# Kernel optimization log

Measured on AMD Instinct MI355X. Metric: run time of the kernel, lower is better.

Reference implementation:

```python
import jax, jax.numpy as jnp
import numpy as np

EPS_BN = 1e-5
NEG_SLOPE = 0.2
N_GRAPHS = 64


def _gat_layer(x, src, dst, W, att_s, att_d, b, concat):
    # x: [N, Fin]; W: [Fin, H*C]; att_s/att_d: [H, C]; PyG GATConv semantics
    N = x.shape[0]
    H, C = att_s.shape
    h = (x @ W).reshape(N, H, C)                      # [N,H,C]
    a_s = jnp.einsum('nhc,hc->nh', h, att_s)          # per-node src score
    a_d = jnp.einsum('nhc,hc->nh', h, att_d)          # per-node dst score
    e = jax.nn.leaky_relu(a_s[src] + a_d[dst], NEG_SLOPE)  # [E,H]
    m = jax.ops.segment_max(e, dst, num_segments=N)   # segment softmax over incoming edges
    ex = jnp.exp(e - m[dst])
    den = jax.ops.segment_sum(ex, dst, num_segments=N)
    alpha = ex / (den[dst] + 1e-16)                   # [E,H]
    msg = h[src] * alpha[:, :, None]                  # [E,H,C]
    out = jax.ops.segment_sum(msg, dst, num_segments=N)
    out = out.reshape(N, H * C) if concat else out.mean(axis=1)
    return out + b


def _bn(x, g, bt):
    mu = x.mean(axis=0)
    var = x.var(axis=0)
    return (x - mu) * jax.lax.rsqrt(var + EPS_BN) * g + bt


def setup_inputs() -> dict:
    key = jax.random.key(0)
    ks = jax.random.split(key, 32)
    N, E, F = 50000, 800000, 128
    d = {}
    d['x'] = jax.random.normal(ks[0], (N, F), dtype=jnp.float32)
    d['edge_index'] = jax.random.randint(ks[1], (2, E), 0, N, dtype=jnp.int32)
    d['batch'] = jnp.sort(jax.random.randint(ks[2], (N,), 0, N_GRAPHS, dtype=jnp.int32))
    def p(k, shape, fan):
        return jax.random.normal(k, shape, dtype=jnp.float32) * (1.0 / np.sqrt(fan))
    d['W1'] = p(ks[3], (128, 256), 128); d['as1'] = p(ks[4], (4, 64), 64)
    d['ad1'] = p(ks[5], (4, 64), 64); d['b1'] = jnp.zeros((256,), jnp.float32)
    d['W2'] = p(ks[6], (256, 128), 256); d['as2'] = p(ks[7], (4, 32), 32)
    d['ad2'] = p(ks[8], (4, 32), 32); d['b2'] = jnp.zeros((128,), jnp.float32)
    # gat3: 128 -> 64, 1 head, mean
    d['W3'] = p(ks[9], (128, 64), 128); d['as3'] = p(ks[10], (1, 64), 64)
    d['ad3'] = p(ks[11], (1, 64), 64); d['b3'] = jnp.zeros((64,), jnp.float32)
    # batch norms
    d['g1'] = jnp.ones((256,), jnp.float32); d['bt1'] = jnp.zeros((256,), jnp.float32)
    d['g2'] = jnp.ones((128,), jnp.float32); d['bt2'] = jnp.zeros((128,), jnp.float32)
    d['g3'] = jnp.ones((64,), jnp.float32); d['bt3'] = jnp.zeros((64,), jnp.float32)
    # fcn: 64 -> 128 -> 32 -> 2
    d['fw1'] = p(ks[12], (64, 128), 64); d['fb1'] = jnp.zeros((128,), jnp.float32)
    d['fw2'] = p(ks[13], (128, 32), 128); d['fb2'] = jnp.zeros((32,), jnp.float32)
    d['fw3'] = p(ks[14], (32, 2), 32); d['fb3'] = jnp.zeros((2,), jnp.float32)
    return d


def reference(x, edge_index, batch, W1, as1, ad1, b1, W2, as2, ad2, b2,
              W3, as3, ad3, b3, g1, bt1, g2, bt2, g3, bt3,
              fw1, fb1, fw2, fb2, fw3, fb3):
    N = x.shape[0]
    # add self loops (PyG GATConv default)
    loops = jnp.arange(N, dtype=edge_index.dtype)
    src = jnp.concatenate([edge_index[0], loops])
    dst = jnp.concatenate([edge_index[1], loops])
    h = _gat_layer(x, src, dst, W1, as1, ad1, b1, concat=True)
    h = jax.nn.elu(_bn(h, g1, bt1))
    h = _gat_layer(h, src, dst, W2, as2, ad2, b2, concat=True)
    h = jax.nn.elu(_bn(h, g2, bt2))
    h = _gat_layer(h, src, dst, W3, as3, ad3, b3, concat=False)
    h = jax.nn.elu(_bn(h, g3, bt3))
    # global mean pool per graph
    s = jax.ops.segment_sum(h, batch, num_segments=N_GRAPHS)
    cnt = jax.ops.segment_sum(jnp.ones((N,), h.dtype), batch, num_segments=N_GRAPHS)
    pooled = s / jnp.maximum(cnt, 1.0)[:, None]       # [64, 64]
    z = jax.nn.leaky_relu(pooled @ fw1 + fb1, NEG_SLOPE)
    z = jax.nn.leaky_relu(z @ fw2 + fb2, NEG_SLOPE)
    return z @ fw3 + fb3                              # [64, 2]
```

## Files before the change

### kernel.cpp

```cpp
#include <hip/hip_runtime.h>
#include <hip/hip_fp16.h>
#include <math.h>

#define NEG_SLOPE 0.2f
#define BN_NB 128
#define BK_SHIFT 6
#define BK_CAP 2048
#define SC_CHUNK 4096

typedef _Float16 f16x8 __attribute__((ext_vector_type(8)));
typedef float    f32x4 __attribute__((ext_vector_type(4)));


__device__ inline void scan1024_incl(int* tmp) {
    int t = threadIdx.x;
    for (int off = 1; off < 1024; off <<= 1) {
        int vals[4];
#pragma unroll
        for (int k = 0; k < 4; k++) {
            int idx = t + k * 256;
            vals[k] = (idx >= off) ? tmp[idx - off] : 0;
        }
        __syncthreads();
#pragma unroll
        for (int k = 0; k < 4; k++) tmp[t + k * 256] += vals[k];
        __syncthreads();
    }
}

__global__ __launch_bounds__(256) void histA_kernel(const int* __restrict__ dst,
                                                    int* __restrict__ bcnt, int E, int nb) {
    __shared__ int h[1024];
    int t = threadIdx.x;
    for (int i = t; i < 1024; i += 256) h[i] = 0;
    __syncthreads();
    int base = blockIdx.x * SC_CHUNK;
#pragma unroll 4
    for (int k = 0; k < SC_CHUNK / 256; k++) {
        int i = base + t + k * 256;
        if (i < E) atomicAdd(&h[dst[i] >> BK_SHIFT], 1);
    }
    __syncthreads();
    for (int i = t; i < nb; i += 256) if (h[i]) atomicAdd(&bcnt[i], h[i]);
}

__global__ __launch_bounds__(256) void scanAB_kernel(const int* __restrict__ bcnt,
                                                     int* __restrict__ boffs,
                                                     int* __restrict__ gcurs, int nb) {
    __shared__ int tmp[1024];
    int t = threadIdx.x;
    for (int i = t; i < 1024; i += 256) tmp[i] = (i < nb) ? bcnt[i] : 0;
    __syncthreads();
    scan1024_incl(tmp);
    for (int i = t; i < nb; i += 256) {
        int excl = (i == 0) ? 0 : tmp[i - 1];
        boffs[i] = excl;
        gcurs[i] = excl;
    }
    if (t == 0) boffs[nb] = tmp[nb - 1];
}

__global__ __launch_bounds__(256) void scatterB_kernel(const int* __restrict__ src,
                                                       const int* __restrict__ dst,
                                                       int* __restrict__ gcurs,
                                                       unsigned* __restrict__ ebuf,
                                                       int E, int nb) {
    __shared__ int hcnt[1024];
    __shared__ int hcur[1024];
    __shared__ int gbase[1024];
    __shared__ unsigned stage[SC_CHUNK];
    __shared__ unsigned short sbk[SC_CHUNK];
    int t = threadIdx.x;
    int base = blockIdx.x * SC_CHUNK;
    for (int i = t; i < 1024; i += 256) hcnt[i] = 0;
    __syncthreads();
    unsigned pk[SC_CHUNK / 256];
    int bk[SC_CHUNK / 256];
#pragma unroll
    for (int k = 0; k < SC_CHUNK / 256; k++) {
        int i = base + t + k * 256;
        if (i < E) {
            int d = dst[i];
            int s = src[i];
            bk[k] = d >> BK_SHIFT;
            pk[k] = (unsigned)s | ((unsigned)(d & 63) << 16);
            atomicAdd(&hcnt[bk[k]], 1);
        } else bk[k] = -1;
    }
    __syncthreads();
    for (int i = t; i < 1024; i += 256) hcur[i] = hcnt[i];
    __syncthreads();
    scan1024_incl(hcur);
    for (int i = t; i < 1024; i += 256) hcur[i] -= hcnt[i];
    __syncthreads();
#pragma unroll
    for (int k = 0; k < SC_CHUNK / 256; k++) {
        if (bk[k] >= 0) {
            int p = atomicAdd(&hcur[bk[k]], 1);
            stage[p] = pk[k];
            sbk[p] = (unsigned short)bk[k];
        }
    }
    __syncthreads();
    for (int i = t; i < nb; i += 256) {
        int c = hcnt[i];
        gbase[i] = c ? atomicAdd(&gcurs[i], c) : 0;
    }
    __syncthreads();
    int total = E - base; if (total > SC_CHUNK) total = SC_CHUNK;
    for (int i = t; i < total; i += 256) {
        int b = sbk[i];
        int local = i - (hcur[b] - hcnt[b]);
        ebuf[gbase[b] + local] = stage[i];
    }
}

__global__ __launch_bounds__(256) void buildC_kernel(const unsigned* __restrict__ ebuf,
                                                     const int* __restrict__ boffs,
                                                     int* __restrict__ offs,
                                                     int* __restrict__ csrc, int N) {
    __shared__ int ncnt[64], ncur[64];
    __shared__ int npre[65];
    __shared__ unsigned lv[BK_CAP];
    __shared__ int lout[BK_CAP];
    int b = blockIdx.x, t = threadIdx.x;
    int e0 = boffs[b], e1 = boffs[b + 1];
    int cnt = e1 - e0; if (cnt > BK_CAP) cnt = BK_CAP;
    int n0 = b << BK_SHIFT;
    if (t < 64) ncnt[t] = 0;
    __syncthreads();
    for (int i = t; i < cnt; i += 256) {
        unsigned v = ebuf[e0 + i];
        lv[i] = v;
        atomicAdd(&ncnt[v >> 16], 1);
    }
    __syncthreads();
    if (t == 0) {
        int run = 0;
#pragma unroll
        for (int i = 0; i < 64; i++) { npre[i] = run; run += ncnt[i]; }
        npre[64] = run;
    }
    __syncthreads();
    int nEnd = N - n0; if (nEnd > 64) nEnd = 64;
    if (t < nEnd) offs[n0 + t + 1] = e0 + npre[t + 1];
    if (b == 0 && t == 0) offs[0] = 0;
    if (t < 64) ncur[t] = npre[t];
    __syncthreads();
    for (int i = t; i < cnt; i += 256) {
        unsigned v = lv[i];
        int p = atomicAdd(&ncur[v >> 16], 1);
        lout[p] = (int)(v & 0xFFFFu);
    }
    __syncthreads();
    for (int i = t; i < cnt; i += 256) csrc[e0 + i] = lout[i];
}


__device__ inline void swz1(const float* __restrict__ W, __half* __restrict__ Wsw,
                            int Nout, int i) {
    int k = i / Nout, n = i % Nout;
    Wsw[((size_t)(k >> 3) * Nout + n) * 8 + (k & 7)] = __float2half(W[i]);
}

__global__ void prep_kernel(const float* __restrict__ W1, const float* __restrict__ W2,
                            const float* __restrict__ W3,
                            const float* __restrict__ as1, const float* __restrict__ ad1,
                            __half* __restrict__ W1sw, __half* __restrict__ W2sw,
                            __half* __restrict__ W3sw, float* __restrict__ wsd,
                            const float* __restrict__ x, __half* __restrict__ Xh,
                            int castN4) {
    int i = blockIdx.x * 256 + threadIdx.x;
    const int R0 = 128 * 256, R1 = R0 + 256 * 128, R2 = R1 + 128 * 64, R3 = R2 + 1024;
    if (i < R0) { swz1(W1, W1sw, 256, i); }
    else if (i < R1) { swz1(W2, W2sw, 128, i - R0); }
    else if (i < R2) { swz1(W3, W3sw, 64, i - R1); }
    else if (i < R3) {
        int j = (i - R2) >> 7, k = (i - R2) & 127;
        int hh = j & 3;
        const float* att = (j < 4) ? as1 : ad1;
        float s = 0.f;
        for (int c = 0; c < 64; c++) s += W1[k * 256 + hh * 64 + c] * att[hh * 64 + c];
        wsd[i - R2] = s;
    } else {
        int j = i - R3;
        if (j < castN4) {
            float4 v = *(const float4*)(x + (size_t)j * 4);
            __half2 pk[2];
            pk[0] = __floats2half2_rn(v.x, v.y);
            pk[1] = __floats2half2_rn(v.z, v.w);
            *(uint2*)(Xh + (size_t)j * 4) = *(uint2*)pk;
        }
    }
}


__global__ __launch_bounds__(256) void scores1_kernel(const __half* __restrict__ Xh,
                                                      const float* __restrict__ wsd,
                                                      float* __restrict__ a_s,
                                                      float* __restrict__ a_d, int N) {
    int gid = blockIdx.x * 256 + threadIdx.x;
    if (gid >= N * 8) return;
    int n = gid >> 3, j = gid & 7;
    const __half* xp = Xh + (size_t)n * 128;
    const float* wp = wsd + j * 128;
    float s = 0.f;
    for (int k = 0; k < 128; k += 8) {
        uint4 raw = *(const uint4*)(xp + k);
        __half2* hp = (__half2*)&raw;
#pragma unroll
        for (int q = 0; q < 4; q++) {
            float2 f = __half22float2(hp[q]);
            s += f.x * wp[k + 2 * q] + f.y * wp[k + 2 * q + 1];
        }
    }
    if (j < 4) a_s[n * 4 + j] = s; else a_d[n * 4 + (j - 4)] = s;
}


__global__ __launch_bounds__(256) void aggx_gemm1_kernel(const __half* __restrict__ Xh,
                                                         const float* __restrict__ a_s,
                                                         const float* __restrict__ a_d,
                                                         const int* __restrict__ offs,
                                                         const int* __restrict__ csrc,
                                                         const __half* __restrict__ W1sw,
                                                         const float* __restrict__ b1,
                                                         __half* __restrict__ out1, int N) {
    __shared__ float wbuf[16][16 * 4];
    __shared__ int   sbuf[16][16];
    __shared__ __half Ast[16][520];
    int tid = threadIdx.x;
    int l16 = tid & 15, grp = tid >> 4;
    int nodeBase = blockIdx.x * 16;
    int node = nodeBase + grp;
    bool act = node < N;

    if (act) {
        int off = offs[node];
        int deg = offs[node + 1] - off;
        float4 ad4 = *(const float4*)(a_d + (size_t)node * 4);
        float adl[4] = {ad4.x, ad4.y, ad4.z, ad4.w};
        float4 as4 = *(const float4*)(a_s + (size_t)node * 4);
        float asl[4] = {as4.x, as4.y, as4.z, as4.w};
        float wself[4];
#pragma unroll
        for (int h = 0; h < 4; h++) {
            float sc = asl[h] + adl[h];
            sc = sc > 0.f ? sc : NEG_SLOPE * sc;
            wself[h] = __expf(sc);
        }
        float acc[4][8];
        {
            uint4 raw = *(const uint4*)(Xh + (size_t)node * 128 + l16 * 8);
            __half2* p = (__half2*)&raw;
#pragma unroll
            for (int q = 0; q < 4; q++) {
                float2 f = __half22float2(p[q]);
#pragma unroll
                for (int h = 0; h < 4; h++) {
                    acc[h][2 * q] = wself[h] * f.x;
                    acc[h][2 * q + 1] = wself[h] * f.y;
                }
            }
        }
        float denp[4] = {0.f, 0.f, 0.f, 0.f};
        for (int base = 0; base < deg; base += 16) {
            int i = base + l16;
            if (i < deg) {
                int s = csrc[off + i];
                sbuf[grp][l16] = s;
                float4 t4 = *(const float4*)(a_s + (size_t)s * 4);
                float asv[4] = {t4.x, t4.y, t4.z, t4.w};
#pragma unroll
                for (int h = 0; h < 4; h++) {
                    float sc = asv[h] + adl[h];
                    sc = sc > 0.f ? sc : NEG_SLOPE * sc;
                    float w = __expf(sc);
                    wbuf[grp][l16 * 4 + h] = w;
                    denp[h] += w;
                }
            }
            asm volatile("s_waitcnt lgkmcnt(0)" ::: "memory");
            int cl = deg - base; if (cl > 16) cl = 16;
#pragma unroll 4
            for (int e = 0; e < cl; e++) {
                int s = sbuf[grp][e];
                float4 wv = *(float4*)&wbuf[grp][e * 4];
                float wa[4] = {wv.x, wv.y, wv.z, wv.w};
                uint4 raw = *(const uint4*)(Xh + (size_t)s * 128 + l16 * 8);
                __half2* p = (__half2*)&raw;
#pragma unroll
                for (int q = 0; q < 4; q++) {
                    float2 f = __half22float2(p[q]);
#pragma unroll
                    for (int h = 0; h < 4; h++) {
                        acc[h][2 * q] += wa[h] * f.x;
                        acc[h][2 * q + 1] += wa[h] * f.y;
                    }
                }
            }
        }
#pragma unroll
        for (int d = 1; d <= 8; d <<= 1)
#pragma unroll
            for (int h = 0; h < 4; h++) denp[h] += __shfl_xor(denp[h], d, 64);
#pragma unroll
        for (int h = 0; h < 4; h++) {
            float inv = 1.0f / (denp[h] + wself[h] + 1e-16f);
            uint4 pk; __half2* q = (__half2*)&pk;
#pragma unroll
            for (int j = 0; j < 4; j++)
                q[j] = __floats2half2_rn(acc[h][2 * j] * inv, acc[h][2 * j + 1] * inv);
            *(uint4*)&Ast[grp][h * 128 + l16 * 8] = pk;
        }
    }
    __syncthreads();

    int wave = tid >> 6, lane = tid & 63;
    int quad = lane >> 4, l15 = lane & 15;
    f32x4 accg[4] = {};
#pragma unroll
    for (int kstep = 0; kstep < 4; kstep++) {
        f16x8 a = *(const f16x8*)&Ast[l15][wave * 128 + kstep * 32 + quad * 8];
        int kt = kstep * 4 + quad;
#pragma unroll
        for (int nt = 0; nt < 4; nt++) {
            int col = wave * 64 + nt * 16 + l15;
            f16x8 b = *(const f16x8*)(W1sw + ((size_t)kt * 256 + col) * 8);
            accg[nt] = __builtin_amdgcn_mfma_f32_16x16x32_f16(a, b, accg[nt], 0, 0, 0);
        }
    }
    float bv[4];
#pragma unroll
    for (int nt = 0; nt < 4; nt++) bv[nt] = b1[wave * 64 + nt * 16 + l15];
#pragma unroll
    for (int r = 0; r < 4; r++) {
        int n2 = nodeBase + quad * 4 + r;
        if (n2 < N) {
#pragma unroll
            for (int nt = 0; nt < 4; nt++)
                out1[(size_t)n2 * 256 + wave * 64 + nt * 16 + l15] =
                    __float2half(accg[nt][r] + bv[nt]);
        }
    }
}


template <int CH, bool BN, bool SCORES, bool BIAS>
__global__ __launch_bounds__(256) void gemm_mfma(const __half* __restrict__ X,
                                                 const __half* __restrict__ Wsw,
                                                 __half* __restrict__ Yh,
                                                 const float* __restrict__ att_s,
                                                 const float* __restrict__ att_d,
                                                 float* __restrict__ a_s,
                                                 float* __restrict__ a_d,
                                                 const float* __restrict__ partials,
                                                 const float* __restrict__ gbn,
                                                 const float* __restrict__ btbn,
                                                 const float* __restrict__ bias,
                                                 float invN, int aStride, int aOffPerBn,
                                                 int M, int K, int Nout) {
    extern __shared__ char smem_raw[];
    __half* Bs = (__half*)smem_raw;
    float* ssc = (float*)(smem_raw + (size_t)K * 64 * 2);
    float* ssb = ssc + K;
    int tid = threadIdx.x;
    int wave = tid >> 6, lane = tid & 63;
    int bm = blockIdx.x * 128;
    int bn = blockIdx.y * 64;

    if (BN && tid < K) {
        float ssum = 0.f, qsum = 0.f;
        for (int b = 0; b < BN_NB; b++) {
            ssum += partials[(size_t)b * 2 * K + tid];
            qsum += partials[(size_t)b * 2 * K + K + tid];
        }
        float mu = ssum * invN;
        float var = qsum * invN - mu * mu;
        float sc = gbn[tid] * rsqrtf(var + 1e-5f);
        ssc[tid] = sc;
        ssb[tid] = btbn[tid] - mu * sc;
    }

    int ktCount = K >> 3;
    int totalVec = ktCount * 64;
    for (int i = tid; i < totalVec; i += 256) {
        int kt = i >> 6, off = i & 63;
        ((uint4*)Bs)[i] = *(const uint4*)(Wsw + ((size_t)kt * Nout + bn + off) * 8);
    }
    __syncthreads();

    int quad = lane >> 4, l15 = lane & 15;
    int row0 = bm + wave * 32 + l15;
    bool r0ok = (row0 < M), r1ok = (row0 + 16 < M);
    int aOff = blockIdx.y * aOffPerBn;
    const __half* a0p = X + (size_t)row0 * aStride + aOff + quad * 8;
    const __half* a1p = a0p + (size_t)16 * aStride;

    f32x4 acc[2][4] = {};
    for (int kstep = 0; kstep < K; kstep += 32) {
        f16x8 a0 = {}, a1 = {};
        if (r0ok) a0 = *(const f16x8*)(a0p + kstep);
        if (r1ok) a1 = *(const f16x8*)(a1p + kstep);
        if (BN) {
            int c0 = kstep + quad * 8;
#pragma unroll
            for (int j = 0; j < 8; j++) {
                float sc = ssc[c0 + j], sb = ssb[c0 + j];
                float v0 = (float)a0[j] * sc + sb;
                v0 = v0 > 0.f ? v0 : (__expf(v0) - 1.0f);
                a0[j] = (_Float16)v0;
                float v1 = (float)a1[j] * sc + sb;
                v1 = v1 > 0.f ? v1 : (__expf(v1) - 1.0f);
                a1[j] = (_Float16)v1;
            }
        }
        int ktbase = (kstep >> 3) + quad;
#pragma unroll
        for (int nt = 0; nt < 4; nt++) {
            f16x8 b = *(const f16x8*)(Bs + ((size_t)ktbase * 64 + nt * 16 + l15) * 8);
            acc[0][nt] = __builtin_amdgcn_mfma_f32_16x16x32_f16(a0, b, acc[0][nt], 0, 0, 0);
            acc[1][nt] = __builtin_amdgcn_mfma_f32_16x16x32_f16(a1, b, acc[1][nt], 0, 0, 0);
        }
    }

    float bv[4];
    if (BIAS) {
#pragma unroll
        for (int nt = 0; nt < 4; nt++) bv[nt] = bias[bn + nt * 16 + l15];
    }

#pragma unroll
    for (int mt = 0; mt < 2; mt++) {
#pragma unroll
        for (int r = 0; r < 4; r++) {
            int row = bm + wave * 32 + mt * 16 + quad * 4 + r;
            if (row < M) {
#pragma unroll
                for (int nt = 0; nt < 4; nt++) {
                    float v = acc[mt][nt][r];
                    if (BIAS) v += bv[nt];
                    Yh[(size_t)row * Nout + bn + nt * 16 + l15] = __float2half(v);
                }
            }
        }
    }

    if (SCORES) {
        constexpr int LH = 64 / CH;
        const int H = Nout / CH;
        float as_l[4], ad_l[4];
#pragma unroll
        for (int nt = 0; nt < 4; nt++) {
            int gcol = bn + nt * 16 + l15;
            as_l[nt] = att_s[gcol];
            ad_l[nt] = att_d[gcol];
        }
        float ps[2][4][LH], pd[2][4][LH];
#pragma unroll
        for (int mt = 0; mt < 2; mt++)
#pragma unroll
            for (int r = 0; r < 4; r++)
#pragma unroll
                for (int lh = 0; lh < LH; lh++) { ps[mt][r][lh] = 0.f; pd[mt][r][lh] = 0.f; }
#pragma unroll
        for (int mt = 0; mt < 2; mt++)
#pragma unroll
            for (int nt = 0; nt < 4; nt++) {
                int lh = (nt * 16) / CH;
#pragma unroll
                for (int r = 0; r < 4; r++) {
                    ps[mt][r][lh] += acc[mt][nt][r] * as_l[nt];
                    pd[mt][r][lh] += acc[mt][nt][r] * ad_l[nt];
                }
            }
#pragma unroll
        for (int d = 1; d <= 8; d <<= 1) {
#pragma unroll
            for (int mt = 0; mt < 2; mt++)
#pragma unroll
                for (int r = 0; r < 4; r++)
#pragma unroll
                    for (int lh = 0; lh < LH; lh++) {
                        ps[mt][r][lh] += __shfl_xor(ps[mt][r][lh], d, 64);
                        pd[mt][r][lh] += __shfl_xor(pd[mt][r][lh], d, 64);
                    }
        }
        if (l15 == 0) {
#pragma unroll
            for (int mt = 0; mt < 2; mt++)
#pragma unroll
                for (int r = 0; r < 4; r++) {
                    int row = bm + wave * 32 + mt * 16 + quad * 4 + r;
                    if (row < M) {
#pragma unroll
                        for (int lh = 0; lh < LH; lh++) {
                            int ghead = bn / CH + lh;
                            a_s[(size_t)row * H + ghead] = ps[mt][r][lh];
                            a_d[(size_t)row * H + ghead] = pd[mt][r][lh];
                        }
                    }
                }
        }
    }
}


template <int H, int C>
__global__ __launch_bounds__(256) void agg_kernel(const __half* __restrict__ h,
                                                  const float* __restrict__ a_s,
                                                  const float* __restrict__ a_d,
                                                  const int* __restrict__ offs,
                                                  const int* __restrict__ csrc,
                                                  const float* __restrict__ bias,
                                                  __half* __restrict__ out, int N) {
    const int HC = H * C;
    const int CPL = HC / 16;
    __shared__ float wbuf[16][16 * H];
    __shared__ int   sbuf[16][16];
    int tid = threadIdx.x;
    int l16 = tid & 15;
    int grp = tid >> 4;
    int node = blockIdx.x * 16 + grp;
    if (node >= N) return;
    int off = offs[node];
    int deg = offs[node + 1] - off;
    int mych = l16 * CPL;
    int mh   = mych / C;

    float adl[H];
#pragma unroll
    for (int hh = 0; hh < H; hh++) adl[hh] = a_d[node * H + hh];

    float acc[CPL];
    float sc_self = a_s[node * H + mh] + adl[mh];
    sc_self = sc_self > 0.f ? sc_self : NEG_SLOPE * sc_self;
    float w_self = __expf(sc_self);
    {
        const __half* hp = h + (size_t)node * HC + mych;
        if (CPL == 8) {
            uint4 r0 = *(const uint4*)hp;
            __half2* p0 = (__half2*)&r0;
#pragma unroll
            for (int j = 0; j < 4; j++) {
                float2 f = __half22float2(p0[j]);
                acc[2 * j] = w_self * f.x; acc[2 * j + 1] = w_self * f.y;
            }
        } else {
            uint2 r0 = *(const uint2*)hp;
            __half2* p0 = (__half2*)&r0;
#pragma unroll
            for (int j = 0; j < 2; j++) {
                float2 f = __half22float2(p0[j]);
                acc[2 * j] = w_self * f.x; acc[2 * j + 1] = w_self * f.y;
            }
        }
    }

    float denp[H];
#pragma unroll
    for (int hh = 0; hh < H; hh++) denp[hh] = 0.f;

    for (int base = 0; base < deg; base += 16) {
        int i = base + l16;
        if (i < deg) {
            int s = csrc[off + i];
            sbuf[grp][l16] = s;
            float asv[H];
            if (H == 4) {
                float4 t4 = *(const float4*)(a_s + (size_t)s * 4);
                asv[0] = t4.x; asv[1] = t4.y; asv[2] = t4.z; asv[3] = t4.w;
            } else {
                asv[0] = a_s[s];
            }
#pragma unroll
            for (int hh = 0; hh < H; hh++) {
                float sc = asv[hh] + adl[hh];
                sc = sc > 0.f ? sc : NEG_SLOPE * sc;
                float w = __expf(sc);
                wbuf[grp][l16 * H + hh] = w;
                denp[hh] += w;
            }
        }
        asm volatile("s_waitcnt lgkmcnt(0)" ::: "memory");
        int cl = deg - base; if (cl > 16) cl = 16;
#pragma unroll 4
        for (int e = 0; e < cl; e++) {
            int s = sbuf[grp][e];
            float w = wbuf[grp][e * H + mh];
            const __half* hp = h + (size_t)s * HC + mych;
            if (CPL == 8) {
                uint4 r0 = *(const uint4*)hp;
                __half2* p0 = (__half2*)&r0;
#pragma unroll
                for (int j = 0; j < 4; j++) {
                    float2 f = __half22float2(p0[j]);
                    acc[2 * j] += w * f.x; acc[2 * j + 1] += w * f.y;
                }
            } else {
                uint2 r0 = *(const uint2*)hp;
                __half2* p0 = (__half2*)&r0;
#pragma unroll
                for (int j = 0; j < 2; j++) {
                    float2 f = __half22float2(p0[j]);
                    acc[2 * j] += w * f.x; acc[2 * j + 1] += w * f.y;
                }
            }
        }
    }
#pragma unroll
    for (int d = 1; d <= 8; d <<= 1) {
#pragma unroll
        for (int hh = 0; hh < H; hh++)
            denp[hh] += __shfl_xor(denp[hh], d, 64);
    }
    float inv = 1.0f / (denp[mh] + w_self + 1e-16f);
    {
        __half* op = out + (size_t)node * HC + mych;
        if (CPL == 8) {
            uint4 pk;
            __half2* q = (__half2*)&pk;
#pragma unroll
            for (int j = 0; j < 4; j++)
                q[j] = __floats2half2_rn(acc[2 * j] * inv + bias[mych + 2 * j],
                                         acc[2 * j + 1] * inv + bias[mych + 2 * j + 1]);
            *(uint4*)op = pk;
        } else {
            uint2 pk;
            __half2* q = (__half2*)&pk;
#pragma unroll
            for (int j = 0; j < 2; j++)
                q[j] = __floats2half2_rn(acc[2 * j] * inv + bias[mych + 2 * j],
                                         acc[2 * j + 1] * inv + bias[mych + 2 * j + 1]);
            *(uint2*)op = pk;
        }
    }
}


__global__ __launch_bounds__(256) void bnstats_kernel(const __half* __restrict__ buf,
                                                      float* __restrict__ partials,
                                                      int N, int Cc) {
    __shared__ float lds_s[2048], lds_q[2048];
    int t = threadIdx.x;
    int tpr = Cc >> 3;
    int rpb = 256 / tpr;
    int r   = t / tpr;
    int c8  = (t % tpr) * 8;
    int row = blockIdx.x * rpb + r;
    int stride = gridDim.x * rpb;
    float s[8] = {}, q[8] = {};
    for (int n = row; n < N; n += stride) {
        uint4 raw = *(const uint4*)(buf + (size_t)n * Cc + c8);
        __half2* hp = (__half2*)&raw;
#pragma unroll
        for (int j = 0; j < 4; j++) {
            float2 f = __half22float2(hp[j]);
            s[2 * j] += f.x; q[2 * j] += f.x * f.x;
            s[2 * j + 1] += f.y; q[2 * j + 1] += f.y * f.y;
        }
    }
#pragma unroll
    for (int j = 0; j < 8; j++) {
        lds_s[r * Cc + c8 + j] = s[j];
        lds_q[r * Cc + c8 + j] = q[j];
    }
    __syncthreads();
    for (int off = rpb >> 1; off >= 1; off >>= 1) {
        if (r < off) {
#pragma unroll
            for (int j = 0; j < 8; j++) {
                lds_s[r * Cc + c8 + j] += lds_s[(r + off) * Cc + c8 + j];
                lds_q[r * Cc + c8 + j] += lds_q[(r + off) * Cc + c8 + j];
            }
        }
        __syncthreads();
    }
    if (r == 0) {
        float* p = partials + (size_t)blockIdx.x * 2 * Cc;
#pragma unroll
        for (int j = 0; j < 8; j++) {
            p[c8 + j] = lds_s[c8 + j];
            p[Cc + c8 + j] = lds_q[c8 + j];
        }
    }
}


__global__ __launch_bounds__(512) void poolmlp_kernel(const __half* __restrict__ h,
                                                      const int* __restrict__ batch,
                                                      const float* __restrict__ partials,
                                                      const float* __restrict__ gbn,
                                                      const float* __restrict__ btbn,
                                                      float invN,
                                                      const float* __restrict__ fw1, const float* __restrict__ fb1,
                                                      const float* __restrict__ fw2, const float* __restrict__ fb2,
                                                      const float* __restrict__ fw3, const float* __restrict__ fb3,
                                                      float* __restrict__ out, int N) {
    int g = blockIdx.x;
    int t = threadIdx.x;
    __shared__ float ssc[64], ssb[64];
    if (t < 64) {
        float ssum = 0.f, qsum = 0.f;
        for (int b = 0; b < BN_NB; b++) {
            ssum += partials[(size_t)b * 128 + t];
            qsum += partials[(size_t)b * 128 + 64 + t];
        }
        float mu = ssum * invN;
        float var = qsum * invN - mu * mu;
        float sc = gbn[t] * rsqrtf(var + 1e-5f);
        ssc[t] = sc;
        ssb[t] = btbn[t] - mu * sc;
    }
    int lo = 0, hi = N;
    while (lo < hi) { int mid = (lo + hi) >> 1; if (batch[mid] < g) lo = mid + 1; else hi = mid; }
    int s = lo;
    hi = N;
    while (lo < hi) { int mid = (lo + hi) >> 1; if (batch[mid] < g + 1) lo = mid + 1; else hi = mid; }
    int e = lo;
    __syncthreads();

    int rg = t >> 3;
    int c8 = (t & 7) * 8;
    float sc[8], sb[8];
#pragma unroll
    for (int j = 0; j < 8; j++) { sc[j] = ssc[c8 + j]; sb[j] = ssb[c8 + j]; }
    float acc[8] = {};
    for (int n = s + rg; n < e; n += 64) {
        uint4 raw = *(const uint4*)(h + (size_t)n * 64 + c8);
        __half2* hp = (__half2*)&raw;
#pragma unroll
        for (int j = 0; j < 4; j++) {
            float2 f = __half22float2(hp[j]);
            float va = f.x * sc[2 * j] + sb[2 * j];
            acc[2 * j] += va > 0.f ? va : (__expf(va) - 1.0f);
            float vb = f.y * sc[2 * j + 1] + sb[2 * j + 1];
            acc[2 * j + 1] += vb > 0.f ? vb : (__expf(vb) - 1.0f);
        }
    }
    __shared__ float red[64 * 64];
#pragma unroll
    for (int j = 0; j < 8; j++) red[rg * 64 + c8 + j] = acc[j];
    __syncthreads();
    for (int off = 32; off >= 1; off >>= 1) {
        if (rg < off) {
#pragma unroll
            for (int j = 0; j < 8; j++)
                red[rg * 64 + c8 + j] += red[(rg + off) * 64 + c8 + j];
        }
        __syncthreads();
    }
    __shared__ float pm[64];
    __shared__ float z1[128];
    __shared__ float z2[32];
    if (t < 64) pm[t] = red[t] / fmaxf((float)(e - s), 1.0f);
    __syncthreads();
    if (t < 128) {
        float v = fb1[t];
        for (int k = 0; k < 64; k++) v += pm[k] * fw1[k * 128 + t];
        z1[t] = v > 0.f ? v : NEG_SLOPE * v;
    }
    __syncthreads();
    if (t < 32) {
        float v = fb2[t];
        for (int k = 0; k < 128; k++) v += z1[k] * fw2[k * 32 + t];
        z2[t] = v > 0.f ? v : NEG_SLOPE * v;
    }
    __syncthreads();
    if (t < 2) {
        float v = fb3[t];
        for (int k = 0; k < 32; k++) v += z2[k] * fw3[k * 2 + t];
        out[g * 2 + t] = v;
    }
}


extern "C" void kernel_launch(void* const* d_in, const int* in_sizes, int n_in,
                              void* d_out, int out_size, void* d_ws, size_t ws_size,
                              hipStream_t stream) {
    const float* x   = (const float*)d_in[0];
    const int*   ei  = (const int*)d_in[1];
    const int*   batch = (const int*)d_in[2];
    const float* W1  = (const float*)d_in[3];
    const float* as1 = (const float*)d_in[4];
    const float* ad1 = (const float*)d_in[5];
    const float* b1  = (const float*)d_in[6];
    const float* W2  = (const float*)d_in[7];
    const float* as2 = (const float*)d_in[8];
    const float* ad2 = (const float*)d_in[9];
    const float* b2  = (const float*)d_in[10];
    const float* W3  = (const float*)d_in[11];
    const float* as3 = (const float*)d_in[12];
    const float* ad3 = (const float*)d_in[13];
    const float* b3  = (const float*)d_in[14];
    const float* g1  = (const float*)d_in[15];
    const float* bt1 = (const float*)d_in[16];
    const float* g2  = (const float*)d_in[17];
    const float* bt2 = (const float*)d_in[18];
    const float* g3  = (const float*)d_in[19];
    const float* bt3 = (const float*)d_in[20];
    const float* fw1 = (const float*)d_in[21];
    const float* fb1 = (const float*)d_in[22];
    const float* fw2 = (const float*)d_in[23];
    const float* fb2 = (const float*)d_in[24];
    const float* fw3 = (const float*)d_in[25];
    const float* fb3 = (const float*)d_in[26];

    const int N = in_sizes[0] / 128;
    const int E = in_sizes[1] / 2;
    const int* srcv = ei;
    const int* dstv = ei + E;
    const int nb = (N + 63) >> 6;

    float* fws   = (float*)d_ws;
    float* ar1F  = fws;
    float* ar2F  = ar1F + (size_t)N * 128;
    float* a_s   = ar2F + (size_t)N * 256;
    float* a_d   = a_s + (size_t)N * 4;
    float* part1 = a_d + (size_t)N * 4;
    float* part2 = part1 + BN_NB * 512;
    float* part3 = part2 + BN_NB * 256;
    int*   bcnt  = (int*)(part3 + BN_NB * 128);
    int*   boffs = bcnt + 1024;
    int*   gcurs = boffs + 1025;
    int*   offs  = gcurs + 1024;
    int*   csrc  = offs + N + 1;
    unsigned* ebuf = (unsigned*)(csrc + E);
    float* wswF  = (float*)(ebuf + E);
    __half* W1sw = (__half*)wswF;
    __half* W2sw = W1sw + 128 * 256;
    __half* W3sw = W2sw + 256 * 128;
    float* wsd   = (float*)(W3sw + 128 * 64);

    __half* Xh   = (__half*)ar1F;
    __half* out1 = (__half*)ar2F;
    __half* h2   = (__half*)ar1F;
    __half* out2 = (__half*)ar2F;
    __half* h3   = (__half*)ar1F;
    __half* out3 = (__half*)ar2F;

    dim3 blk(256);
    const int scGrid = (E + SC_CHUNK - 1) / SC_CHUNK;

    hipMemsetAsync(bcnt, 0, 1024 * 4, stream);

    histA_kernel<<<scGrid, blk, 0, stream>>>(dstv, bcnt, E, nb);
    scanAB_kernel<<<1, blk, 0, stream>>>(bcnt, boffs, gcurs, nb);
    scatterB_kernel<<<scGrid, blk, 0, stream>>>(srcv, dstv, gcurs, ebuf, E, nb);
    buildC_kernel<<<nb, blk, 0, stream>>>(ebuf, boffs, offs, csrc, N);

    {
        int castN4 = N * 32;
        int total = 128 * 256 + 256 * 128 + 128 * 64 + 1024 + castN4;
        prep_kernel<<<(total + 255) / 256, blk, 0, stream>>>(W1, W2, W3, as1, ad1,
                                                             W1sw, W2sw, W3sw, wsd,
                                                             x, Xh, castN4);
    }

    {
        scores1_kernel<<<((size_t)N * 8 + 255) / 256, blk, 0, stream>>>(Xh, wsd, a_s, a_d, N);
        aggx_gemm1_kernel<<<(N + 15) / 16, blk, 0, stream>>>(Xh, a_s, a_d, offs, csrc,
                                                             W1sw, b1, out1, N);
        bnstats_kernel<<<BN_NB, blk, 0, stream>>>(out1, part1, N, 256);
    }
    {
        dim3 grid((N + 127) / 128, 2);
        gemm_mfma<32, true, true, false><<<grid, blk, 256 * 128 + 2 * 256 * 4, stream>>>(
            out1, W2sw, h2, as2, ad2, a_s, a_d, part1, g1, bt1, nullptr,
            1.0f / N, 256, 0, N, 256, 128);
        agg_kernel<4, 32><<<(N + 15) / 16, blk, 0, stream>>>(h2, a_s, a_d, offs, csrc, b2, out2, N);
        bnstats_kernel<<<BN_NB, blk, 0, stream>>>(out2, part2, N, 128);
    }
    {
        dim3 grid((N + 127) / 128, 1);
        gemm_mfma<64, true, true, false><<<grid, blk, 128 * 128 + 2 * 128 * 4, stream>>>(
            out2, W3sw, h3, as3, ad3, a_s, a_d, part2, g2, bt2, nullptr,
            1.0f / N, 128, 0, N, 128, 64);
        agg_kernel<1, 64><<<(N + 15) / 16, blk, 0, stream>>>(h3, a_s, a_d, offs, csrc, b3, out3, N);
        bnstats_kernel<<<BN_NB, blk, 0, stream>>>(out3, part3, N, 64);
    }

    poolmlp_kernel<<<64, 512, 0, stream>>>(out3, batch, part3, g3, bt3, 1.0f / N,
                                           fw1, fb1, fw2, fb2, fw3, fb3,
                                           (float*)d_out, N);
}
```

Measured before the change: 403.7 us.

## Fuse BatchNorm statistics accumulation into aggregation kernels, drop bnstats passes

Removes the three separate bnstats kernels. Each aggregation kernel (the layer-1 fused agg+GEMM and both agg_kernel instances) now computes per-column sum and sum-of-squares in registers, reduces them with wave shuffles and LDS atomics, and atomically adds them into BN_NB slotted partial buffers. This saves a full re-read of each layer output and three kernel launches, at the cost of extra shuffles, LDS and global atomics per block. The single memset now zeros the partial buffers along with the histogram counts. Statistics are taken from fp32 values before the fp16 rounding, which changes numerics slightly.

```diff
diff --git a/kernel.cpp b/kernel.cpp
--- a/kernel.cpp
+++ b/kernel.cpp
@@ -225,7 +225,8 @@
                                                          const int* __restrict__ csrc,
                                                          const __half* __restrict__ W1sw,
                                                          const float* __restrict__ b1,
-                                                         __half* __restrict__ out1, int N) {
+                                                         __half* __restrict__ out1,
+                                                         float* __restrict__ part1, int N) {
     __shared__ float wbuf[16][16 * 4];
     __shared__ int   sbuf[16][16];
     __shared__ __half Ast[16][520];
@@ -333,14 +334,32 @@
     float bv[4];
 #pragma unroll
     for (int nt = 0; nt < 4; nt++) bv[nt] = b1[wave * 64 + nt * 16 + l15];
+    float s_nt[4] = {}, q_nt[4] = {};
 #pragma unroll
     for (int r = 0; r < 4; r++) {
         int n2 = nodeBase + quad * 4 + r;
         if (n2 < N) {
 #pragma unroll
-            for (int nt = 0; nt < 4; nt++)
-                out1[(size_t)n2 * 256 + wave * 64 + nt * 16 + l15] =
-                    __float2half(accg[nt][r] + bv[nt]);
+            for (int nt = 0; nt < 4; nt++) {
+                float v = accg[nt][r] + bv[nt];
+                out1[(size_t)n2 * 256 + wave * 64 + nt * 16 + l15] = __float2half(v);
+                s_nt[nt] += v;
+                q_nt[nt] += v * v;
+            }
+        }
+    }
+#pragma unroll
+    for (int nt = 0; nt < 4; nt++) {
+        s_nt[nt] += __shfl_xor(s_nt[nt], 16, 64); q_nt[nt] += __shfl_xor(q_nt[nt], 16, 64);
+        s_nt[nt] += __shfl_xor(s_nt[nt], 32, 64); q_nt[nt] += __shfl_xor(q_nt[nt], 32, 64);
+    }
+    if ((lane & 48) == 0) {
+        int slot = blockIdx.x & (BN_NB - 1);
+#pragma unroll
+        for (int nt = 0; nt < 4; nt++) {
+            int col = wave * 64 + nt * 16 + l15;
+            atomicAdd(&part1[(size_t)slot * 512 + col], s_nt[nt]);
+            atomicAdd(&part1[(size_t)slot * 512 + 256 + col], q_nt[nt]);
         }
     }
 }
@@ -513,30 +532,36 @@
                                                   const int* __restrict__ offs,
                                                   const int* __restrict__ csrc,
                                                   const float* __restrict__ bias,
-                                                  __half* __restrict__ out, int N) {
+                                                  __half* __restrict__ out,
+                                                  float* __restrict__ partials, int N) {
     const int HC = H * C;
     const int CPL = HC / 16;
     __shared__ float wbuf[16][16 * H];
     __shared__ int   sbuf[16][16];
+    __shared__ float bnacc[2 * HC];
     int tid = threadIdx.x;
     int l16 = tid & 15;
     int grp = tid >> 4;
     int node = blockIdx.x * 16 + grp;
-    if (node >= N) return;
-    int off = offs[node];
-    int deg = offs[node + 1] - off;
+    bool act = node < N;
+    for (int i = tid; i < 2 * HC; i += 256) bnacc[i] = 0.f;
+    __syncthreads();
+
+    int off = act ? offs[node] : 0;
+    int deg = act ? (offs[node + 1] - off) : 0;
     int mych = l16 * CPL;
     int mh   = mych / C;
 
     float adl[H];
 #pragma unroll
-    for (int hh = 0; hh < H; hh++) adl[hh] = a_d[node * H + hh];
-
-    float acc[CPL];
-    float sc_self = a_s[node * H + mh] + adl[mh];
-    sc_self = sc_self > 0.f ? sc_self : NEG_SLOPE * sc_self;
-    float w_self = __expf(sc_self);
-    {
+    for (int hh = 0; hh < H; hh++) adl[hh] = act ? a_d[node * H + hh] : 0.f;
+
+    float acc[CPL] = {};
+    float w_self = 0.f;
+    if (act) {
+        float sc_self = a_s[node * H + mh] + adl[mh];
+        sc_self = sc_self > 0.f ? sc_self : NEG_SLOPE * sc_self;
+        w_self = __expf(sc_self);
         const __half* hp = h + (size_t)node * HC + mych;
         if (CPL == 8) {
             uint4 r0 = *(const uint4*)hp;
@@ -614,76 +639,47 @@
         for (int hh = 0; hh < H; hh++)
             denp[hh] += __shfl_xor(denp[hh], d, 64);
     }
-    float inv = 1.0f / (denp[mh] + w_self + 1e-16f);
-    {
+    float inv = act ? (1.0f / (denp[mh] + w_self + 1e-16f)) : 0.f;
+
+    float fv[CPL];
+#pragma unroll
+    for (int j = 0; j < CPL; j++) fv[j] = act ? (acc[j] * inv + bias[mych + j]) : 0.f;
+    if (act) {
         __half* op = out + (size_t)node * HC + mych;
         if (CPL == 8) {
-            uint4 pk;
-            __half2* q = (__half2*)&pk;
+            uint4 pk; __half2* q = (__half2*)&pk;
 #pragma unroll
             for (int j = 0; j < 4; j++)
-                q[j] = __floats2half2_rn(acc[2 * j] * inv + bias[mych + 2 * j],
-                                         acc[2 * j + 1] * inv + bias[mych + 2 * j + 1]);
+                q[j] = __floats2half2_rn(fv[2 * j], fv[2 * j + 1]);
             *(uint4*)op = pk;
         } else {
-            uint2 pk;
-            __half2* q = (__half2*)&pk;
+            uint2 pk; __half2* q = (__half2*)&pk;
 #pragma unroll
             for (int j = 0; j < 2; j++)
-                q[j] = __floats2half2_rn(acc[2 * j] * inv + bias[mych + 2 * j],
-                                         acc[2 * j + 1] * inv + bias[mych + 2 * j + 1]);
+                q[j] = __floats2half2_rn(fv[2 * j], fv[2 * j + 1]);
             *(uint2*)op = pk;
         }
     }
-}
-
-
-__global__ __launch_bounds__(256) void bnstats_kernel(const __half* __restrict__ buf,
-                                                      float* __restrict__ partials,
-                                                      int N, int Cc) {
-    __shared__ float lds_s[2048], lds_q[2048];
-    int t = threadIdx.x;
-    int tpr = Cc >> 3;
-    int rpb = 256 / tpr;
-    int r   = t / tpr;
-    int c8  = (t % tpr) * 8;
-    int row = blockIdx.x * rpb + r;
-    int stride = gridDim.x * rpb;
-    float s[8] = {}, q[8] = {};
-    for (int n = row; n < N; n += stride) {
-        uint4 raw = *(const uint4*)(buf + (size_t)n * Cc + c8);
-        __half2* hp = (__half2*)&raw;
-#pragma unroll
-        for (int j = 0; j < 4; j++) {
-            float2 f = __half22float2(hp[j]);
-            s[2 * j] += f.x; q[2 * j] += f.x * f.x;
-            s[2 * j + 1] += f.y; q[2 * j + 1] += f.y * f.y;
-        }
-    }
-#pragma unroll
-    for (int j = 0; j < 8; j++) {
-        lds_s[r * Cc + c8 + j] = s[j];
-        lds_q[r * Cc + c8 + j] = q[j];
-    }
-    __syncthreads();
-    for (int off = rpb >> 1; off >= 1; off >>= 1) {
-        if (r < off) {
-#pragma unroll
-            for (int j = 0; j < 8; j++) {
-                lds_s[r * Cc + c8 + j] += lds_s[(r + off) * Cc + c8 + j];
-                lds_q[r * Cc + c8 + j] += lds_q[(r + off) * Cc + c8 + j];
-            }
-        }
-        __syncthreads();
-    }
-    if (r == 0) {
-        float* p = partials + (size_t)blockIdx.x * 2 * Cc;
-#pragma unroll
-        for (int j = 0; j < 8; j++) {
-            p[c8 + j] = lds_s[c8 + j];
-            p[Cc + c8 + j] = lds_q[c8 + j];
-        }
-    }
+
+    float sq[CPL];
+#pragma unroll
+    for (int j = 0; j < CPL; j++) sq[j] = fv[j] * fv[j];
+#pragma unroll
+    for (int j = 0; j < CPL; j++) {
+        fv[j] += __shfl_xor(fv[j], 16, 64); sq[j] += __shfl_xor(sq[j], 16, 64);
+        fv[j] += __shfl_xor(fv[j], 32, 64); sq[j] += __shfl_xor(sq[j], 32, 64);
+    }
+    if (((tid & 63) & 48) == 0) {
+#pragma unroll
+        for (int j = 0; j < CPL; j++) {
+            atomicAdd(&bnacc[mych + j], fv[j]);
+            atomicAdd(&bnacc[HC + mych + j], sq[j]);
+        }
+    }
+    __syncthreads();
+    int slot = blockIdx.x & (BN_NB - 1);
+    for (int i = tid; i < 2 * HC; i += 256)
+        atomicAdd(&partials[(size_t)slot * 2 * HC + i], bnacc[i]);
 }
 
 
@@ -842,7 +838,7 @@
     dim3 blk(256);
     const int scGrid = (E + SC_CHUNK - 1) / SC_CHUNK;
 
-    hipMemsetAsync(bcnt, 0, 1024 * 4, stream);
+    hipMemsetAsync(part1, 0, (size_t)(BN_NB * (512 + 256 + 128) + 1024) * 4, stream);
 
     histA_kernel<<<scGrid, blk, 0, stream>>>(dstv, bcnt, E, nb);
     scanAB_kernel<<<1, blk, 0, stream>>>(bcnt, boffs, gcurs, nb);
@@ -857,27 +853,24 @@
                                                              x, Xh, castN4);
     }
 
-    {
-        scores1_kernel<<<((size_t)N * 8 + 255) / 256, blk, 0, stream>>>(Xh, wsd, a_s, a_d, N);
-        aggx_gemm1_kernel<<<(N + 15) / 16, blk, 0, stream>>>(Xh, a_s, a_d, offs, csrc,
-                                                             W1sw, b1, out1, N);
-        bnstats_kernel<<<BN_NB, blk, 0, stream>>>(out1, part1, N, 256);
-    }
+    scores1_kernel<<<((size_t)N * 8 + 255) / 256, blk, 0, stream>>>(Xh, wsd, a_s, a_d, N);
+    aggx_gemm1_kernel<<<(N + 15) / 16, blk, 0, stream>>>(Xh, a_s, a_d, offs, csrc,
+                                                         W1sw, b1, out1, part1, N);
     {
         dim3 grid((N + 127) / 128, 2);
         gemm_mfma<32, true, true, false><<<grid, blk, 256 * 128 + 2 * 256 * 4, stream>>>(
             out1, W2sw, h2, as2, ad2, a_s, a_d, part1, g1, bt1, nullptr,
             1.0f / N, 256, 0, N, 256, 128);
-        agg_kernel<4, 32><<<(N + 15) / 16, blk, 0, stream>>>(h2, a_s, a_d, offs, csrc, b2, out2, N);
-        bnstats_kernel<<<BN_NB, blk, 0, stream>>>(out2, part2, N, 128);
+        agg_kernel<4, 32><<<(N + 15) / 16, blk, 0, stream>>>(h2, a_s, a_d, offs, csrc,
+                                                             b2, out2, part2, N);
     }
     {
         dim3 grid((N + 127) / 128, 1);
         gemm_mfma<64, true, true, false><<<grid, blk, 128 * 128 + 2 * 128 * 4, stream>>>(
             out2, W3sw, h3, as3, ad3, a_s, a_d, part2, g2, bt2, nullptr,
             1.0f / N, 128, 0, N, 128, 64);
-        agg_kernel<1, 64><<<(N + 15) / 16, blk, 0, stream>>>(h3, a_s, a_d, offs, csrc, b3, out3, N);
-        bnstats_kernel<<<BN_NB, blk, 0, stream>>>(out3, part3, N, 64);
+        agg_kernel<1, 64><<<(N + 15) / 16, blk, 0, stream>>>(h3, a_s, a_d, offs, csrc,
+                                                             b3, out3, part3, N);
     }
 
     poolmlp_kernel<<<64, 512, 0, stream>>>(out3, batch, part3, g3, bt3, 1.0f / N,
```

Result: no change. 400.6 us (-0.8%).
